# Performance work log

Hardware: AMD Instinct MI355X
Metric: run time of the kernel (lower is better)

The kernel has to match this reference:

```python
import jax, jax.numpy as jnp
import numpy as np

B, L, N, C = 64, 12, 4096, 3
FD, HD, OUT = 32, 64, 12
TID, DIW, TD = 288, 7, 16
STEPS = 4
EMB = 10  # node embedding dim for learned adjacency


def setup_inputs() -> dict:
    key = jax.random.key(0)
    ks = jax.random.split(key, 16)
    g = lambda i, shape, s=0.05: jax.random.normal(ks[i], shape, dtype=jnp.float32) * s
    z = lambda n: jnp.zeros((n,), jnp.float32)
    return {
        "history_data": jax.random.uniform(ks[0], (B, L, N, C), dtype=jnp.float32),
        "future_data": jnp.zeros((B, L, N, 1), jnp.float32),
        "batch_seen": 0,
        "epoch": 0,
        "train": 1,
        "tid_emb": g(1, (TID, TD)),
        "diw_emb": g(2, (DIW, TD)),
        "t2f_w": g(3, (2 * TD, FD)), "t2f_b": z(FD),
        "enc_w1": g(4, (L * C, HD)), "enc_b1": z(HD),
        "enc_w2": g(5, (HD, FD)), "enc_b2": z(FD),
        "node_emb": g(6, (N, EMB), 1.0),
        "pde_w1": g(7, (FD, HD)), "pde_b1": z(HD),
        "pde_w2": g(8, (HD, FD)), "pde_b2": z(FD),
        "ss_win": g(9, (FD, FD)), "ss_wst": g(10, (FD, FD)), "ss_b": z(FD),
        "ss_wout": g(11, (FD, FD)), "ss_bout": z(FD),
        "dec_w1": g(12, (FD, HD)), "dec_b1": z(HD),
        "dec_w2": g(13, (HD, OUT)), "dec_b2": z(OUT),
        "pde_mix": jnp.array(0.5, jnp.float32),
    }


def reference(history_data, future_data, batch_seen, epoch, train,
              tid_emb, diw_emb, t2f_w, t2f_b,
              enc_w1, enc_b1, enc_w2, enc_b2,
              node_emb,
              pde_w1, pde_b1, pde_w2, pde_b2,
              ss_win, ss_wst, ss_b, ss_wout, ss_bout,
              dec_w1, dec_b1, dec_w2, dec_b2, pde_mix):
    # --- encoder: per-node MLP over flattened (L, C) history ---
    x = history_data[..., :C]                                    # [B,L,N,C]
    x = jnp.transpose(x, (0, 2, 1, 3)).reshape(B, N, L * C)      # [B,N,L*C]
    field = jnp.maximum(x @ enc_w1 + enc_b1, 0.0) @ enc_w2 + enc_b2  # [B,N,FD]

    # --- temporal field bias from last-step tid/diw ---
    tid_idx = jnp.clip((history_data[:, -1, :, 1] * TID).astype(jnp.int32), 0, TID - 1)
    diw_idx = jnp.clip((history_data[:, -1, :, 2] * DIW).astype(jnp.int32), 0, DIW - 1)
    temp = jnp.concatenate([tid_emb[tid_idx], diw_emb[diw_idx]], axis=-1)  # [B,N,2*TD]
    field = field + temp @ t2f_w + t2f_b

    # --- learned adjacency for graph Laplacian (L = I - A) ---
    A = jax.nn.softmax(jnp.maximum(node_emb @ node_emb.T, 0.0), axis=-1)  # [N,N]

    alpha = jax.nn.sigmoid(pde_mix)
    dt = 1.0 / STEPS
    state = jnp.zeros_like(field)
    for _ in range(STEPS):  # fixed small unroll over PDE steps
        L_F = jnp.einsum('nm,bmf->bnf', A, field) - field         # (A - I) F
        N_F = jnp.maximum(field @ pde_w1 + pde_b1, 0.0) @ pde_w2 + pde_b2
        fe = field + (alpha * L_F + (1.0 - alpha) * N_F) * dt
        state = jnp.tanh(fe @ ss_win + state @ ss_wst + ss_b)     # state-space update
        field = fe + state @ ss_wout + ss_bout

    # --- decoder: per-node MLP to output horizon ---
    pred = jnp.maximum(field @ dec_w1 + dec_b1, 0.0) @ dec_w2 + dec_b2  # [B,N,OUT]
    return jnp.transpose(pred, (0, 2, 1))[..., None]              # [B,OUT,N,1]
```

## Files before the change

### kernel.cpp

```cpp
#include <hip/hip_runtime.h>

#define BATCH 64
#define LHIST 12
#define NNODE 4096
#define CCH   3
#define FD    32
#define HD    64
#define OUTD  12
#define TIDN  288
#define DIWN  7
#define TDD   16
#define EMBD  10
#define MROWS 2048
#define KDIM  4096
#define MTOT  (BATCH * NNODE)

typedef __attribute__((ext_vector_type(8))) short bf16x8;
typedef __attribute__((ext_vector_type(4))) float f32x4;

union BF8U { bf16x8 v; unsigned short s[8]; };

__device__ __forceinline__ unsigned short f2b(float f) {
    union { float f; unsigned u; } v; v.f = f;
    unsigned r = v.u + 0x7fffu + ((v.u >> 16) & 1u);
    return (unsigned short)(r >> 16);
}

__device__ __forceinline__ float b2f(unsigned short u) {
    union { unsigned u; float f; } v; v.u = (unsigned)u << 16; return v.f;
}

__device__ __forceinline__ float fast_tanh(float x) {
    x = fminf(fmaxf(x, -15.f), 15.f);
    const float e = __expf(2.f * x);
    return (e - 1.f) / (e + 1.f);
}

__device__ __forceinline__ bf16x8 ldsfrag(const unsigned short* p) {
    return *(const bf16x8*)p;
}

__device__ __forceinline__ bf16x8 pack8(float4 a, float4 b) {
    BF8U u;
    u.s[0] = f2b(a.x); u.s[1] = f2b(a.y); u.s[2] = f2b(a.z); u.s[3] = f2b(a.w);
    u.s[4] = f2b(b.x); u.s[5] = f2b(b.y); u.s[6] = f2b(b.z); u.s[7] = f2b(b.w);
    return u.v;
}

__global__ __launch_bounds__(256) void build_A(const float* __restrict__ emb,
                                               unsigned short* __restrict__ A) {
    const int n = blockIdx.x;
    const int tid = threadIdx.x;
    __shared__ float sc[NNODE];
    __shared__ float red[256];
    float e[EMBD];
#pragma unroll
    for (int c = 0; c < EMBD; c++) e[c] = emb[(size_t)n * EMBD + c];
    float mx = 0.f;
    for (int m = tid; m < NNODE; m += 256) {
        float s = 0.f;
#pragma unroll
        for (int c = 0; c < EMBD; c++) s += e[c] * emb[(size_t)m * EMBD + c];
        s = fmaxf(s, 0.f);
        sc[m] = s;
        mx = fmaxf(mx, s);
    }
    red[tid] = mx;
    __syncthreads();
    for (int off = 128; off > 0; off >>= 1) {
        if (tid < off) red[tid] = fmaxf(red[tid], red[tid + off]);
        __syncthreads();
    }
    mx = red[0];
    __syncthreads();
    float sum = 0.f;
    for (int m = tid; m < NNODE; m += 256) {
        float v = expf(sc[m] - mx);
        sc[m] = v;
        sum += v;
    }
    red[tid] = sum;
    __syncthreads();
    for (int off = 128; off > 0; off >>= 1) {
        if (tid < off) red[tid] += red[tid + off];
        __syncthreads();
    }
    const float inv = 1.f / red[0];
    for (int m = tid; m < NNODE; m += 256)
        A[(size_t)n * NNODE + m] = f2b(sc[m] * inv);
}

__global__ __launch_bounds__(256, 2) void encoder(const float* __restrict__ hist,
                                                  const float* __restrict__ tid_emb,
                                                  const float* __restrict__ diw_emb,
                                                  const float* __restrict__ t2f_w,
                                                  const float* __restrict__ t2f_b,
                                                  const float* __restrict__ enc_w1,
                                                  const float* __restrict__ enc_b1,
                                                  const float* __restrict__ enc_w2,
                                                  const float* __restrict__ enc_b2,
                                                  float* __restrict__ field,
                                                  unsigned short* __restrict__ fT) {
    const int gid = blockIdx.x * 256 + threadIdx.x;
    const int b = gid >> 12;
    const int n = gid & (NNODE - 1);
    const float* hb = hist + ((size_t)b * LHIST * NNODE + n) * CCH;
    float x[LHIST * CCH];
#pragma unroll
    for (int l = 0; l < LHIST; l++) {
        x[l * 3 + 0] = hb[(size_t)l * NNODE * CCH + 0];
        x[l * 3 + 1] = hb[(size_t)l * NNODE * CCH + 1];
        x[l * 3 + 2] = hb[(size_t)l * NNODE * CCH + 2];
    }
    float f[FD];
#pragma unroll
    for (int o = 0; o < FD; o++) f[o] = enc_b2[o] + t2f_b[o];
    for (int j = 0; j < HD; j++) {
        float h = enc_b1[j];
#pragma unroll
        for (int k = 0; k < LHIST * CCH; k++) h += x[k] * enc_w1[k * HD + j];
        h = fmaxf(h, 0.f);
#pragma unroll
        for (int o = 0; o < FD; o++) f[o] += h * enc_w2[j * FD + o];
    }
    const int ti = min(max((int)(x[11 * 3 + 1] * 288.0f), 0), TIDN - 1);
    const int di = min(max((int)(x[11 * 3 + 2] * 7.0f), 0), DIWN - 1);
    for (int g = 0; g < TDD; g++) {
        const float tg = tid_emb[ti * TDD + g];
        const float dg = diw_emb[di * TDD + g];
#pragma unroll
        for (int o = 0; o < FD; o++)
            f[o] += tg * t2f_w[g * FD + o] + dg * t2f_w[(TDD + g) * FD + o];
    }
#pragma unroll
    for (int o4 = 0; o4 < FD / 4; o4++) {
        float4 v = {f[o4 * 4 + 0], f[o4 * 4 + 1], f[o4 * 4 + 2], f[o4 * 4 + 3]};
        *(float4*)&field[(size_t)gid * FD + o4 * 4] = v;
    }
#pragma unroll
    for (int o = 0; o < FD; o++)
        fT[(size_t)(b * FD + o) * NNODE + n] = f2b(f[o]);
}

__global__ __launch_bounds__(256) void gemm_bt(const unsigned short* __restrict__ X,
                                               const unsigned short* __restrict__ Y,
                                               unsigned short* __restrict__ Cp) {
    constexpr int K = KDIM;
    constexpr int KS = KDIM / 2;
    constexpr int BK = 32;
    __shared__ __align__(16) unsigned short Xs[2][128 * BK];
    __shared__ __align__(16) unsigned short Ys[2][128 * BK];
    const int tid = threadIdx.x;
    const int wave = tid >> 6;
    const int lane = tid & 63;

    const int l = blockIdx.x + 16 * blockIdx.y;
    const int xcd = l & 7;
    const int rem = l >> 3;
    const int by = xcd * 4 + (rem & 3);
    const int bx = rem >> 2;
    const int i0 = bx * 128;
    const int j0 = by * 128;
    const int k0 = blockIdx.z * KS;
    unsigned short* C = Cp + (size_t)blockIdx.z * MTOT * FD;

    const int wi = (wave >> 1) * 64;
    const int wj = (wave & 1) * 64;

    const int lrow = lane >> 2;
    const int gcol = (lane & 3) * 8;
    const int scol = ((lane & 3) ^ ((lane >> 3) & 3)) * 8;

    const unsigned short* Xg = X + (size_t)(i0 + wave * 32 + lrow) * K + k0 + gcol;
    const unsigned short* Yg = Y + (size_t)(j0 + wave * 32 + lrow) * K + k0 + gcol;
    const int ldoff0 = (wave * 32 + lrow) * BK + scol;
    const int ldoff1 = (wave * 32 + 16 + lrow) * BK + scol;

    const f32x4 zero = {0.f, 0.f, 0.f, 0.f};
    f32x4 acc[4][4];
#pragma unroll
    for (int a = 0; a < 4; a++)
#pragma unroll
        for (int b = 0; b < 4; b++) acc[a][b] = zero;

    const int fr = lane & 15;
    const int q = lane >> 4;
    const int kq = (q ^ ((fr >> 1) & 3)) * 8;

    uint4 rx0 = *(const uint4*)(Xg);
    uint4 rx1 = *(const uint4*)(Xg + 16 * K);
    uint4 ry0 = *(const uint4*)(Yg);
    uint4 ry1 = *(const uint4*)(Yg + 16 * K);
    *(uint4*)&Xs[0][ldoff0] = rx0;
    *(uint4*)&Xs[0][ldoff1] = rx1;
    *(uint4*)&Ys[0][ldoff0] = ry0;
    *(uint4*)&Ys[0][ldoff1] = ry1;
    __syncthreads();

    int p = 0;
    for (int kt = 0; kt < KS; kt += BK) {
        const bool more = (kt + BK < KS);
        if (more) {
            rx0 = *(const uint4*)(Xg + kt + BK);
            rx1 = *(const uint4*)(Xg + kt + BK + 16 * K);
            ry0 = *(const uint4*)(Yg + kt + BK);
            ry1 = *(const uint4*)(Yg + kt + BK + 16 * K);
        }
        bf16x8 fa[4], fb[4];
#pragma unroll
        for (int t = 0; t < 4; t++)
            fa[t] = *(const bf16x8*)&Xs[p][(wi + t * 16 + fr) * BK + kq];
#pragma unroll
        for (int t = 0; t < 4; t++)
            fb[t] = *(const bf16x8*)&Ys[p][(wj + t * 16 + fr) * BK + kq];
#pragma unroll
        for (int mi = 0; mi < 4; mi++)
#pragma unroll
            for (int ni = 0; ni < 4; ni++)
                acc[mi][ni] = __builtin_amdgcn_mfma_f32_16x16x32_bf16(
                    fa[mi], fb[ni], acc[mi][ni], 0, 0, 0);
        if (more) {
            const int np = p ^ 1;
            *(uint4*)&Xs[np][ldoff0] = rx0;
            *(uint4*)&Xs[np][ldoff1] = rx1;
            *(uint4*)&Ys[np][ldoff0] = ry0;
            *(uint4*)&Ys[np][ldoff1] = ry1;
            __syncthreads();
            p = np;
        }
    }

    const int r0 = q * 4;
#pragma unroll
    for (int mi = 0; mi < 4; mi++) {
#pragma unroll
        for (int ni = 0; ni < 4; ni++) {
            const int R0 = i0 + wi + mi * 16 + r0;
            const int col = j0 + wj + ni * 16 + fr;
            const size_t addr = ((size_t)(R0 >> 5) * NNODE + col) * FD + (R0 & 31);
            ushort4 pk = {f2b(acc[mi][ni][0]), f2b(acc[mi][ni][1]),
                          f2b(acc[mi][ni][2]), f2b(acc[mi][ni][3])};
            *(ushort4*)&C[addr] = pk;
        }
    }
}

#define HPAD 72
#define FPAD 40
__global__ __launch_bounds__(256, 2) void step_mfma(const unsigned short* __restrict__ Ct0,
                                                    const unsigned short* __restrict__ Ct1,
                                                    float* __restrict__ field,
                                                    unsigned short* __restrict__ state,
                                                    unsigned short* __restrict__ fT,
                                                    const float* __restrict__ pde_w1,
                                                    const float* __restrict__ pde_b1,
                                                    const float* __restrict__ pde_w2,
                                                    const float* __restrict__ pde_b2,
                                                    const float* __restrict__ ss_win,
                                                    const float* __restrict__ ss_wst,
                                                    const float* __restrict__ ss_b,
                                                    const float* __restrict__ ss_wout,
                                                    const float* __restrict__ ss_bout,
                                                    const float* __restrict__ pde_mix,
                                                    const float* __restrict__ dec_w1,
                                                    const float* __restrict__ dec_b1,
                                                    const float* __restrict__ dec_w2,
                                                    const float* __restrict__ dec_b2,
                                                    float* __restrict__ out,
                                                    int first, int last) {
    __shared__ __align__(16) unsigned short W1T[HD * FD];
    __shared__ __align__(16) unsigned short W2T[FD * HD];
    __shared__ __align__(16) unsigned short WinT[FD * FD];
    __shared__ __align__(16) unsigned short WstT[FD * FD];
    __shared__ __align__(16) unsigned short WoutT[FD * FD];
    __shared__ __align__(16) unsigned short Wd1T[HD * FD];
    __shared__ __align__(16) unsigned short Wd2T[16 * HD];
    __shared__ __align__(16) unsigned short Hs[4 * 64 * HPAD];
    __shared__ __align__(16) unsigned short Fs[4 * 64 * FPAD];

    const int tid = threadIdx.x;
    for (int i = tid; i < HD * FD; i += 256) W1T[(i & 63) * FD + (i >> 6)] = f2b(pde_w1[i]);
    for (int i = tid; i < HD * FD; i += 256) W2T[(i & 31) * HD + (i >> 5)] = f2b(pde_w2[i]);
    for (int i = tid; i < FD * FD; i += 256) {
        WinT [(i & 31) * FD + (i >> 5)] = f2b(ss_win[i]);
        WstT [(i & 31) * FD + (i >> 5)] = f2b(ss_wst[i]);
        WoutT[(i & 31) * FD + (i >> 5)] = f2b(ss_wout[i]);
    }
    if (last) {
        for (int i = tid; i < HD * FD; i += 256)
            Wd1T[(i & 63) * FD + (i >> 6)] = f2b(dec_w1[i]);
        for (int i = tid; i < 16 * HD; i += 256) {
            const int o = i >> 6, j = i & 63;
            Wd2T[i] = (o < OUTD) ? f2b(dec_w2[j * OUTD + o]) : (unsigned short)0;
        }
    }
    __syncthreads();

    const int wv = tid >> 6;
    const int lane = tid & 63;
    const int ln = lane & 15;
    const int q = lane >> 4;
    const int kq = q * 8;
    const int r0 = q * 4;
    const int mw = blockIdx.x * 256 + wv * 64;
    const int b = mw >> 12;
    const int n0 = mw & (NNODE - 1);
    unsigned short* Hw = &Hs[wv * 64 * HPAD];
    unsigned short* Fw = &Fs[wv * 64 * FPAD];

    const float alpha = 1.f / (1.f + __expf(-pde_mix[0]));
    const float dt = 0.25f;

    bf16x8 w1f[4], w2f[2][2], winf[2], wstf[2], woutf[2];
#pragma unroll
    for (int nj = 0; nj < 4; nj++) w1f[nj] = ldsfrag(&W1T[(nj * 16 + ln) * FD + kq]);
#pragma unroll
    for (int nf = 0; nf < 2; nf++) {
#pragma unroll
        for (int kk = 0; kk < 2; kk++)
            w2f[nf][kk] = ldsfrag(&W2T[(nf * 16 + ln) * HD + kk * 32 + kq]);
        winf[nf]  = ldsfrag(&WinT [(nf * 16 + ln) * FD + kq]);
        wstf[nf]  = ldsfrag(&WstT [(nf * 16 + ln) * FD + kq]);
        woutf[nf] = ldsfrag(&WoutT[(nf * 16 + ln) * FD + kq]);
    }

    float b1v[4], b2v[2], bsv[2], bov[2];
#pragma unroll
    for (int nj = 0; nj < 4; nj++) b1v[nj] = pde_b1[nj * 16 + ln];
#pragma unroll
    for (int nf = 0; nf < 2; nf++) {
        b2v[nf] = pde_b2[nf * 16 + ln];
        bsv[nf] = ss_b[nf * 16 + ln];
        bov[nf] = ss_bout[nf * 16 + ln];
    }

    bf16x8 fA[4], stA[4];
#pragma unroll
    for (int mi = 0; mi < 4; mi++) {
        const float4* fp = (const float4*)&field[(size_t)(mw + mi * 16 + ln) * FD + kq];
        fA[mi] = pack8(fp[0], fp[1]);
    }
    if (!first) {
#pragma unroll
        for (int mi = 0; mi < 4; mi++)
            stA[mi] = *(const bf16x8*)&state[(size_t)(mw + mi * 16 + ln) * FD + kq];
    }

    const f32x4 zero = {0.f, 0.f, 0.f, 0.f};

    f32x4 hc[4][4];
#pragma unroll
    for (int mi = 0; mi < 4; mi++)
#pragma unroll
        for (int nj = 0; nj < 4; nj++)
            hc[mi][nj] = __builtin_amdgcn_mfma_f32_16x16x32_bf16(fA[mi], w1f[nj], zero, 0, 0, 0);
#pragma unroll
    for (int mi = 0; mi < 4; mi++)
#pragma unroll
        for (int nj = 0; nj < 4; nj++)
#pragma unroll
            for (int r = 0; r < 4; r++)
                Hw[(mi * 16 + r0 + r) * HPAD + nj * 16 + ln] =
                    f2b(fmaxf(hc[mi][nj][r] + b1v[nj], 0.f));

    float fld[4][2][4], ctv[4][2][4];
#pragma unroll
    for (int mi = 0; mi < 4; mi++)
#pragma unroll
        for (int nf = 0; nf < 2; nf++)
#pragma unroll
            for (int r = 0; r < 4; r++) {
                const size_t idx = (size_t)(mw + mi * 16 + r0 + r) * FD + nf * 16 + ln;
                fld[mi][nf][r] = field[idx];
                ctv[mi][nf][r] = b2f(Ct0[idx]) + b2f(Ct1[idx]);
            }

    bf16x8 hA[4][2];
#pragma unroll
    for (int mi = 0; mi < 4; mi++)
#pragma unroll
        for (int kk = 0; kk < 2; kk++)
            hA[mi][kk] = ldsfrag(&Hw[(mi * 16 + ln) * HPAD + kk * 32 + kq]);
    f32x4 nc[4][2];
#pragma unroll
    for (int mi = 0; mi < 4; mi++)
#pragma unroll
        for (int nf = 0; nf < 2; nf++) {
            f32x4 a = __builtin_amdgcn_mfma_f32_16x16x32_bf16(hA[mi][0], w2f[nf][0], zero, 0, 0, 0);
            nc[mi][nf] = __builtin_amdgcn_mfma_f32_16x16x32_bf16(hA[mi][1], w2f[nf][1], a, 0, 0, 0);
        }

    float fe[4][2][4];
#pragma unroll
    for (int mi = 0; mi < 4; mi++)
#pragma unroll
        for (int nf = 0; nf < 2; nf++)
#pragma unroll
            for (int r = 0; r < 4; r++) {
                const float nfv = nc[mi][nf][r] + b2v[nf];
                const float fv = fld[mi][nf][r];
                fe[mi][nf][r] = fv + (alpha * (ctv[mi][nf][r] - fv) + (1.f - alpha) * nfv) * dt;
                Fw[(mi * 16 + r0 + r) * FPAD + nf * 16 + ln] = f2b(fe[mi][nf][r]);
            }

    bf16x8 feA[4];
#pragma unroll
    for (int mi = 0; mi < 4; mi++) feA[mi] = ldsfrag(&Fw[(mi * 16 + ln) * FPAD + kq]);
    f32x4 sc_[4][2];
#pragma unroll
    for (int mi = 0; mi < 4; mi++)
#pragma unroll
        for (int nf = 0; nf < 2; nf++) {
            f32x4 a = __builtin_amdgcn_mfma_f32_16x16x32_bf16(feA[mi], winf[nf], zero, 0, 0, 0);
            if (!first)
                a = __builtin_amdgcn_mfma_f32_16x16x32_bf16(stA[mi], wstf[nf], a, 0, 0, 0);
            sc_[mi][nf] = a;
        }
    float sval[4][2][4];
#pragma unroll
    for (int mi = 0; mi < 4; mi++)
#pragma unroll
        for (int nf = 0; nf < 2; nf++)
#pragma unroll
            for (int r = 0; r < 4; r++)
                sval[mi][nf][r] = fast_tanh(sc_[mi][nf][r] + bsv[nf]);
#pragma unroll
    for (int mi = 0; mi < 4; mi++)
#pragma unroll
        for (int nf = 0; nf < 2; nf++)
#pragma unroll
            for (int r = 0; r < 4; r++)
                Fw[(mi * 16 + r0 + r) * FPAD + nf * 16 + ln] = f2b(sval[mi][nf][r]);

    bf16x8 SA[4];
#pragma unroll
    for (int mi = 0; mi < 4; mi++) SA[mi] = ldsfrag(&Fw[(mi * 16 + ln) * FPAD + kq]);
    float fnew[4][2][4];
#pragma unroll
    for (int mi = 0; mi < 4; mi++)
#pragma unroll
        for (int nf = 0; nf < 2; nf++) {
            f32x4 oc = __builtin_amdgcn_mfma_f32_16x16x32_bf16(SA[mi], woutf[nf], zero, 0, 0, 0);
#pragma unroll
            for (int r = 0; r < 4; r++)
                fnew[mi][nf][r] = fe[mi][nf][r] + oc[r] + bov[nf];
        }

    if (!last) {
#pragma unroll
        for (int mi = 0; mi < 4; mi++) {
#pragma unroll
            for (int nf = 0; nf < 2; nf++) {
#pragma unroll
                for (int r = 0; r < 4; r++) {
                    const size_t idx = (size_t)(mw + mi * 16 + r0 + r) * FD + nf * 16 + ln;
                    field[idx] = fnew[mi][nf][r];
                    state[idx] = f2b(sval[mi][nf][r]);
                }
                ushort4 pk = {f2b(fnew[mi][nf][0]), f2b(fnew[mi][nf][1]),
                              f2b(fnew[mi][nf][2]), f2b(fnew[mi][nf][3])};
                const size_t ft_addr = (size_t)(b * FD + nf * 16 + ln) * NNODE + n0 + mi * 16 + r0;
                *(ushort4*)&fT[ft_addr] = pk;
            }
        }
    } else {
        bf16x8 wd1f[4], wd2f[2];
#pragma unroll
        for (int nj = 0; nj < 4; nj++) wd1f[nj] = ldsfrag(&Wd1T[(nj * 16 + ln) * FD + kq]);
#pragma unroll
        for (int kk = 0; kk < 2; kk++) wd2f[kk] = ldsfrag(&Wd2T[ln * HD + kk * 32 + kq]);
        float db1v[4];
#pragma unroll
        for (int nj = 0; nj < 4; nj++) db1v[nj] = dec_b1[nj * 16 + ln];
        const float db2v = (ln < OUTD) ? dec_b2[ln] : 0.f;

#pragma unroll
        for (int mi = 0; mi < 4; mi++)
#pragma unroll
            for (int nf = 0; nf < 2; nf++)
#pragma unroll
                for (int r = 0; r < 4; r++)
                    Fw[(mi * 16 + r0 + r) * FPAD + nf * 16 + ln] = f2b(fnew[mi][nf][r]);
        bf16x8 fnA[4];
#pragma unroll
        for (int mi = 0; mi < 4; mi++) fnA[mi] = ldsfrag(&Fw[(mi * 16 + ln) * FPAD + kq]);

        f32x4 h2[4][4];
#pragma unroll
        for (int mi = 0; mi < 4; mi++)
#pragma unroll
            for (int nj = 0; nj < 4; nj++)
                h2[mi][nj] = __builtin_amdgcn_mfma_f32_16x16x32_bf16(fnA[mi], wd1f[nj], zero, 0, 0, 0);
#pragma unroll
        for (int mi = 0; mi < 4; mi++)
#pragma unroll
            for (int nj = 0; nj < 4; nj++)
#pragma unroll
                for (int r = 0; r < 4; r++)
                    Hw[(mi * 16 + r0 + r) * HPAD + nj * 16 + ln] =
                        f2b(fmaxf(h2[mi][nj][r] + db1v[nj], 0.f));
        bf16x8 h2A[4][2];
#pragma unroll
        for (int mi = 0; mi < 4; mi++)
#pragma unroll
            for (int kk = 0; kk < 2; kk++)
                h2A[mi][kk] = ldsfrag(&Hw[(mi * 16 + ln) * HPAD + kk * 32 + kq]);
#pragma unroll
        for (int mi = 0; mi < 4; mi++) {
            f32x4 a = __builtin_amdgcn_mfma_f32_16x16x32_bf16(h2A[mi][0], wd2f[0], zero, 0, 0, 0);
            a = __builtin_amdgcn_mfma_f32_16x16x32_bf16(h2A[mi][1], wd2f[1], a, 0, 0, 0);
            if (ln < OUTD) {
                float4 v = {a[0] + db2v, a[1] + db2v, a[2] + db2v, a[3] + db2v};
                *(float4*)&out[(size_t)(b * OUTD + ln) * NNODE + n0 + mi * 16 + r0] = v;
            }
        }
    }
}

extern "C" void kernel_launch(void* const* d_in, const int* in_sizes, int n_in,
                              void* d_out, int out_size, void* d_ws, size_t ws_size,
                              hipStream_t stream) {
    (void)in_sizes; (void)n_in; (void)out_size; (void)ws_size;
    const float* hist    = (const float*)d_in[0];
    const float* tid_emb = (const float*)d_in[5];
    const float* diw_emb = (const float*)d_in[6];
    const float* t2f_w   = (const float*)d_in[7];
    const float* t2f_b   = (const float*)d_in[8];
    const float* enc_w1  = (const float*)d_in[9];
    const float* enc_b1  = (const float*)d_in[10];
    const float* enc_w2  = (const float*)d_in[11];
    const float* enc_b2  = (const float*)d_in[12];
    const float* node_emb= (const float*)d_in[13];
    const float* pde_w1  = (const float*)d_in[14];
    const float* pde_b1  = (const float*)d_in[15];
    const float* pde_w2  = (const float*)d_in[16];
    const float* pde_b2  = (const float*)d_in[17];
    const float* ss_win  = (const float*)d_in[18];
    const float* ss_wst  = (const float*)d_in[19];
    const float* ss_b    = (const float*)d_in[20];
    const float* ss_wout = (const float*)d_in[21];
    const float* ss_bout = (const float*)d_in[22];
    const float* dec_w1  = (const float*)d_in[23];
    const float* dec_b1  = (const float*)d_in[24];
    const float* dec_w2  = (const float*)d_in[25];
    const float* dec_b2  = (const float*)d_in[26];
    const float* pde_mix = (const float*)d_in[27];

    char* w = (char*)d_ws;
    unsigned short* A_bf = (unsigned short*)w;  w += (size_t)KDIM * KDIM * 2;
    unsigned short* fT   = (unsigned short*)w;  w += (size_t)MROWS * KDIM * 2;
    float* field = (float*)w;                   w += (size_t)MTOT * FD * 4;
    unsigned short* state = (unsigned short*)w; w += (size_t)MTOT * FD * 2;
    unsigned short* Cp    = (unsigned short*)w; w += (size_t)2 * MTOT * FD * 2;

    build_A<<<NNODE, 256, 0, stream>>>(node_emb, A_bf);
    encoder<<<(BATCH * NNODE) / 256, 256, 0, stream>>>(hist, tid_emb, diw_emb, t2f_w,
                                                       t2f_b, enc_w1, enc_b1, enc_w2,
                                                       enc_b2, field, fT);
    for (int s = 0; s < 4; s++) {
        gemm_bt<<<dim3(16, 32, 2), 256, 0, stream>>>(fT, A_bf, Cp);
        step_mfma<<<MTOT / 256, 256, 0, stream>>>(
            Cp, Cp + (size_t)MTOT * FD, field, state, fT, pde_w1, pde_b1, pde_w2,
            pde_b2, ss_win, ss_wst, ss_b, ss_wout, ss_bout, pde_mix,
            dec_w1, dec_b1, dec_w2, dec_b2, (float*)d_out,
            s == 0 ? 1 : 0, s == 3 ? 1 : 0);
    }
}
```

Measured before the change: 732.0 us.

## Fuse graph GEMM with PDE step epilogue for first three steps

Adds a gemm_step kernel that computes the full-K A·F product for a 128x128 tile and runs the PDE/state-space update in its epilogue. The result is staged through shared memory instead of bf16 split-K partials in global memory, which removes a separate step kernel launch and the partial round trip for three of the four steps. fT is ping-ponged between two buffers because the fused kernel writes the next transposed field while other blocks still read the current one. The last step keeps split-K plus step_mfma with the decoder. The GEMM main loop is also unrolled by two with a deeper register prefetch. The costs are half as many blocks in the fused GEMM (no split-K), which may hurt occupancy, and a larger shared-memory footprint.

```diff
diff --git a/kernel.cpp b/kernel.cpp
--- a/kernel.cpp
+++ b/kernel.cpp
@@ -142,14 +142,318 @@
         fT[(size_t)(b * FD + o) * NNODE + n] = f2b(f[o]);
 }
 
+#define TPAD 36
+#define QHP  72
+#define QFP  40
+__global__ __launch_bounds__(256) void gemm_step(const unsigned short* __restrict__ X,
+                                                 const unsigned short* __restrict__ Y,
+                                                 float* __restrict__ field,
+                                                 unsigned short* __restrict__ state,
+                                                 unsigned short* __restrict__ fTo,
+                                                 const float* __restrict__ pde_w1,
+                                                 const float* __restrict__ pde_b1,
+                                                 const float* __restrict__ pde_w2,
+                                                 const float* __restrict__ pde_b2,
+                                                 const float* __restrict__ ss_win,
+                                                 const float* __restrict__ ss_wst,
+                                                 const float* __restrict__ ss_b,
+                                                 const float* __restrict__ ss_wout,
+                                                 const float* __restrict__ ss_bout,
+                                                 const float* __restrict__ pde_mix,
+                                                 int first) {
+    constexpr int K = KDIM;
+    constexpr int BK = 32;
+    __shared__ __align__(16) unsigned short SM0[512 * TPAD];
+    __shared__ __align__(16) unsigned short W1T[HD * FD];
+    __shared__ __align__(16) unsigned short W2T[FD * HD];
+    __shared__ __align__(16) unsigned short WinT[FD * FD];
+    __shared__ __align__(16) unsigned short WstT[FD * FD];
+    __shared__ __align__(16) unsigned short WoutT[FD * FD];
+    __shared__ __align__(16) unsigned short Hs[4 * 32 * QHP];
+    __shared__ __align__(16) unsigned short Fs[4 * 32 * QFP];
+
+    const int tid = threadIdx.x;
+    const int wave = tid >> 6;
+    const int lane = tid & 63;
+
+    for (int i = tid; i < HD * FD; i += 256) W1T[(i & 63) * FD + (i >> 6)] = f2b(pde_w1[i]);
+    for (int i = tid; i < HD * FD; i += 256) W2T[(i & 31) * HD + (i >> 5)] = f2b(pde_w2[i]);
+    for (int i = tid; i < FD * FD; i += 256) {
+        WinT [(i & 31) * FD + (i >> 5)] = f2b(ss_win[i]);
+        WstT [(i & 31) * FD + (i >> 5)] = f2b(ss_wst[i]);
+        WoutT[(i & 31) * FD + (i >> 5)] = f2b(ss_wout[i]);
+    }
+
+    const int l = blockIdx.x + 16 * blockIdx.y;
+    const int xcd = l & 7;
+    const int rem = l >> 3;
+    const int by = xcd * 4 + (rem & 3);
+    const int bx = rem >> 2;
+    const int i0 = bx * 128;
+    const int j0 = by * 128;
+    const int b0 = i0 >> 5;
+
+    const int wi = (wave >> 1) * 64;
+    const int wj = (wave & 1) * 64;
+
+    const int lrow = lane >> 2;
+    const int gcol = (lane & 3) * 8;
+    const int scol = ((lane & 3) ^ ((lane >> 3) & 3)) * 8;
+
+    const unsigned short* Xg = X + (size_t)(i0 + wave * 32 + lrow) * K + gcol;
+    const unsigned short* Yg = Y + (size_t)(j0 + wave * 32 + lrow) * K + gcol;
+    unsigned short* Xs = SM0;
+    unsigned short* Ys = SM0 + 8192;
+    const int ld0 = (wave * 32 + lrow) * BK + scol;
+    const int ld1 = (wave * 32 + 16 + lrow) * BK + scol;
+
+    const f32x4 zero = {0.f, 0.f, 0.f, 0.f};
+    f32x4 acc[4][4];
+#pragma unroll
+    for (int a = 0; a < 4; a++)
+#pragma unroll
+        for (int b = 0; b < 4; b++) acc[a][b] = zero;
+
+    const int fr = lane & 15;
+    const int q = lane >> 4;
+    const int kq8 = (q ^ ((fr >> 1) & 3)) * 8;
+
+#define GS_COMPUTE(P)                                                              \
+    {                                                                              \
+        bf16x8 fa[4], fb[4];                                                       \
+        _Pragma("unroll") for (int t = 0; t < 4; t++)                              \
+            fa[t] = *(const bf16x8*)&Xs[(P) * 4096 + (wi + t * 16 + fr) * BK + kq8]; \
+        _Pragma("unroll") for (int t = 0; t < 4; t++)                              \
+            fb[t] = *(const bf16x8*)&Ys[(P) * 4096 + (wj + t * 16 + fr) * BK + kq8]; \
+        _Pragma("unroll") for (int mi = 0; mi < 4; mi++)                           \
+            _Pragma("unroll") for (int ni = 0; ni < 4; ni++)                       \
+                acc[mi][ni] = __builtin_amdgcn_mfma_f32_16x16x32_bf16(             \
+                    fa[mi], fb[ni], acc[mi][ni], 0, 0, 0);                         \
+    }
+
+    uint4 ax0 = *(const uint4*)(Xg);
+    uint4 ax1 = *(const uint4*)(Xg + 16 * K);
+    uint4 ay0 = *(const uint4*)(Yg);
+    uint4 ay1 = *(const uint4*)(Yg + 16 * K);
+    uint4 bx0 = *(const uint4*)(Xg + BK);
+    uint4 bx1 = *(const uint4*)(Xg + BK + 16 * K);
+    uint4 by0 = *(const uint4*)(Yg + BK);
+    uint4 by1 = *(const uint4*)(Yg + BK + 16 * K);
+    *(uint4*)&Xs[ld0] = ax0; *(uint4*)&Xs[ld1] = ax1;
+    *(uint4*)&Ys[ld0] = ay0; *(uint4*)&Ys[ld1] = ay1;
+    __syncthreads();
+
+    int p = 0;
+    for (int kt = 0; kt < K; kt += 2 * BK) {
+        if (kt + 2 * BK < K) {
+            ax0 = *(const uint4*)(Xg + kt + 2 * BK);
+            ax1 = *(const uint4*)(Xg + kt + 2 * BK + 16 * K);
+            ay0 = *(const uint4*)(Yg + kt + 2 * BK);
+            ay1 = *(const uint4*)(Yg + kt + 2 * BK + 16 * K);
+        }
+        GS_COMPUTE(p);
+        {
+            const int np = p ^ 1;
+            *(uint4*)&Xs[np * 4096 + ld0] = bx0; *(uint4*)&Xs[np * 4096 + ld1] = bx1;
+            *(uint4*)&Ys[np * 4096 + ld0] = by0; *(uint4*)&Ys[np * 4096 + ld1] = by1;
+            __syncthreads();
+        }
+        if (kt + 3 * BK < K) {
+            bx0 = *(const uint4*)(Xg + kt + 3 * BK);
+            bx1 = *(const uint4*)(Xg + kt + 3 * BK + 16 * K);
+            by0 = *(const uint4*)(Yg + kt + 3 * BK);
+            by1 = *(const uint4*)(Yg + kt + 3 * BK + 16 * K);
+        }
+        GS_COMPUTE(p ^ 1);
+        if (kt + 2 * BK < K) {
+            *(uint4*)&Xs[p * 4096 + ld0] = ax0; *(uint4*)&Xs[p * 4096 + ld1] = ax1;
+            *(uint4*)&Ys[p * 4096 + ld0] = ay0; *(uint4*)&Ys[p * 4096 + ld1] = ay1;
+            __syncthreads();
+        }
+    }
+#undef GS_COMPUTE
+
+    __syncthreads();
+    unsigned short* T = SM0;
+    const int r0 = q * 4;
+#pragma unroll
+    for (int mi = 0; mi < 4; mi++) {
+#pragma unroll
+        for (int ni = 0; ni < 4; ni++) {
+            const int R0 = i0 + wi + mi * 16 + r0;
+            const int nl = wj + ni * 16 + fr;
+            ushort4 pk = {f2b(acc[mi][ni][0]), f2b(acc[mi][ni][1]),
+                          f2b(acc[mi][ni][2]), f2b(acc[mi][ni][3])};
+            *(ushort4*)&T[((((R0 >> 5) & 3) << 7) + nl) * TPAD + (R0 & 31)] = pk;
+        }
+    }
+    __syncthreads();
+
+    const int ln = fr;
+    const int kq = q * 8;
+    unsigned short* Hw = &Hs[wave * 32 * QHP];
+    unsigned short* Fw = &Fs[wave * 32 * QFP];
+    const float alpha = 1.f / (1.f + __expf(-pde_mix[0]));
+    const float dt = 0.25f;
+
+    bf16x8 w1f[4], w2f[2][2], winf[2], wstf[2], woutf[2];
+#pragma unroll
+    for (int nj = 0; nj < 4; nj++) w1f[nj] = ldsfrag(&W1T[(nj * 16 + ln) * FD + kq]);
+#pragma unroll
+    for (int nf = 0; nf < 2; nf++) {
+#pragma unroll
+        for (int kk = 0; kk < 2; kk++)
+            w2f[nf][kk] = ldsfrag(&W2T[(nf * 16 + ln) * HD + kk * 32 + kq]);
+        winf[nf]  = ldsfrag(&WinT [(nf * 16 + ln) * FD + kq]);
+        wstf[nf]  = ldsfrag(&WstT [(nf * 16 + ln) * FD + kq]);
+        woutf[nf] = ldsfrag(&WoutT[(nf * 16 + ln) * FD + kq]);
+    }
+    float b1v[4], b2v[2], bsv[2], bov[2];
+#pragma unroll
+    for (int nj = 0; nj < 4; nj++) b1v[nj] = pde_b1[nj * 16 + ln];
+#pragma unroll
+    for (int nf = 0; nf < 2; nf++) {
+        b2v[nf] = pde_b2[nf * 16 + ln];
+        bsv[nf] = ss_b[nf * 16 + ln];
+        bov[nf] = ss_bout[nf * 16 + ln];
+    }
+
+    for (int qtr = 0; qtr < 4; qtr++) {
+        const int lb = wave * 128 + qtr * 32;
+        const int bb = lb >> 7;
+        const int nl0 = lb & 127;
+        const int bg = b0 + bb;
+        const int mwg = (bg << 12) + j0 + nl0;
+
+        bf16x8 fA[2], stA[2];
+#pragma unroll
+        for (int mi = 0; mi < 2; mi++) {
+            const float4* fp = (const float4*)&field[(size_t)(mwg + mi * 16 + ln) * FD + kq];
+            fA[mi] = pack8(fp[0], fp[1]);
+        }
+        if (!first) {
+#pragma unroll
+            for (int mi = 0; mi < 2; mi++)
+                stA[mi] = *(const bf16x8*)&state[(size_t)(mwg + mi * 16 + ln) * FD + kq];
+        }
+
+        f32x4 hc[2][4];
+#pragma unroll
+        for (int mi = 0; mi < 2; mi++)
+#pragma unroll
+            for (int nj = 0; nj < 4; nj++)
+                hc[mi][nj] = __builtin_amdgcn_mfma_f32_16x16x32_bf16(fA[mi], w1f[nj], zero, 0, 0, 0);
+#pragma unroll
+        for (int mi = 0; mi < 2; mi++)
+#pragma unroll
+            for (int nj = 0; nj < 4; nj++)
+#pragma unroll
+                for (int r = 0; r < 4; r++)
+                    Hw[(mi * 16 + r0 + r) * QHP + nj * 16 + ln] =
+                        f2b(fmaxf(hc[mi][nj][r] + b1v[nj], 0.f));
+
+        float fld[2][2][4], ctv[2][2][4];
+#pragma unroll
+        for (int mi = 0; mi < 2; mi++)
+#pragma unroll
+            for (int nf = 0; nf < 2; nf++)
+#pragma unroll
+                for (int r = 0; r < 4; r++) {
+                    const size_t idx = (size_t)(mwg + mi * 16 + r0 + r) * FD + nf * 16 + ln;
+                    fld[mi][nf][r] = field[idx];
+                    ctv[mi][nf][r] = b2f(T[(lb + mi * 16 + r0 + r) * TPAD + nf * 16 + ln]);
+                }
+
+        bf16x8 hA[2][2];
+#pragma unroll
+        for (int mi = 0; mi < 2; mi++)
+#pragma unroll
+            for (int kk = 0; kk < 2; kk++)
+                hA[mi][kk] = ldsfrag(&Hw[(mi * 16 + ln) * QHP + kk * 32 + kq]);
+        f32x4 nc[2][2];
+#pragma unroll
+        for (int mi = 0; mi < 2; mi++)
+#pragma unroll
+            for (int nf = 0; nf < 2; nf++) {
+                f32x4 a = __builtin_amdgcn_mfma_f32_16x16x32_bf16(hA[mi][0], w2f[nf][0], zero, 0, 0, 0);
+                nc[mi][nf] = __builtin_amdgcn_mfma_f32_16x16x32_bf16(hA[mi][1], w2f[nf][1], a, 0, 0, 0);
+            }
+
+        float fe[2][2][4];
+#pragma unroll
+        for (int mi = 0; mi < 2; mi++)
+#pragma unroll
+            for (int nf = 0; nf < 2; nf++)
+#pragma unroll
+                for (int r = 0; r < 4; r++) {
+                    const float nfv = nc[mi][nf][r] + b2v[nf];
+                    const float fv = fld[mi][nf][r];
+                    fe[mi][nf][r] = fv + (alpha * (ctv[mi][nf][r] - fv) + (1.f - alpha) * nfv) * dt;
+                    Fw[(mi * 16 + r0 + r) * QFP + nf * 16 + ln] = f2b(fe[mi][nf][r]);
+                }
+
+        bf16x8 feA[2];
+#pragma unroll
+        for (int mi = 0; mi < 2; mi++) feA[mi] = ldsfrag(&Fw[(mi * 16 + ln) * QFP + kq]);
+        f32x4 sc_[2][2];
+#pragma unroll
+        for (int mi = 0; mi < 2; mi++)
+#pragma unroll
+            for (int nf = 0; nf < 2; nf++) {
+                f32x4 a = __builtin_amdgcn_mfma_f32_16x16x32_bf16(feA[mi], winf[nf], zero, 0, 0, 0);
+                if (!first)
+                    a = __builtin_amdgcn_mfma_f32_16x16x32_bf16(stA[mi], wstf[nf], a, 0, 0, 0);
+                sc_[mi][nf] = a;
+            }
+        float sval[2][2][4];
+#pragma unroll
+        for (int mi = 0; mi < 2; mi++)
+#pragma unroll
+            for (int nf = 0; nf < 2; nf++)
+#pragma unroll
+                for (int r = 0; r < 4; r++)
+                    sval[mi][nf][r] = fast_tanh(sc_[mi][nf][r] + bsv[nf]);
+#pragma unroll
+        for (int mi = 0; mi < 2; mi++)
+#pragma unroll
+            for (int nf = 0; nf < 2; nf++)
+#pragma unroll
+                for (int r = 0; r < 4; r++)
+                    Fw[(mi * 16 + r0 + r) * QFP + nf * 16 + ln] = f2b(sval[mi][nf][r]);
+
+        bf16x8 SA[2];
+#pragma unroll
+        for (int mi = 0; mi < 2; mi++) SA[mi] = ldsfrag(&Fw[(mi * 16 + ln) * QFP + kq]);
+#pragma unroll
+        for (int mi = 0; mi < 2; mi++) {
+#pragma unroll
+            for (int nf = 0; nf < 2; nf++) {
+                f32x4 oc = __builtin_amdgcn_mfma_f32_16x16x32_bf16(SA[mi], woutf[nf], zero, 0, 0, 0);
+                float fnew[4];
+#pragma unroll
+                for (int r = 0; r < 4; r++) {
+                    fnew[r] = fe[mi][nf][r] + oc[r] + bov[nf];
+                    const size_t idx = (size_t)(mwg + mi * 16 + r0 + r) * FD + nf * 16 + ln;
+                    field[idx] = fnew[r];
+                    state[idx] = f2b(sval[mi][nf][r]);
+                }
+                ushort4 pk = {f2b(fnew[0]), f2b(fnew[1]), f2b(fnew[2]), f2b(fnew[3])};
+                const size_t fta = (size_t)(bg * FD + nf * 16 + ln) * NNODE
+                                 + j0 + nl0 + mi * 16 + r0;
+                *(ushort4*)&fTo[fta] = pk;
+            }
+        }
+    }
+}
+
 __global__ __launch_bounds__(256) void gemm_bt(const unsigned short* __restrict__ X,
                                                const unsigned short* __restrict__ Y,
                                                unsigned short* __restrict__ Cp) {
     constexpr int K = KDIM;
     constexpr int KS = KDIM / 2;
     constexpr int BK = 32;
-    __shared__ __align__(16) unsigned short Xs[2][128 * BK];
-    __shared__ __align__(16) unsigned short Ys[2][128 * BK];
+    __shared__ __align__(16) unsigned short Xs[2 * 4096];
+    __shared__ __align__(16) unsigned short Ys[2 * 4096];
     const int tid = threadIdx.x;
     const int wave = tid >> 6;
     const int lane = tid & 63;
@@ -173,8 +477,8 @@
 
     const unsigned short* Xg = X + (size_t)(i0 + wave * 32 + lrow) * K + k0 + gcol;
     const unsigned short* Yg = Y + (size_t)(j0 + wave * 32 + lrow) * K + k0 + gcol;
-    const int ldoff0 = (wave * 32 + lrow) * BK + scol;
-    const int ldoff1 = (wave * 32 + 16 + lrow) * BK + scol;
+    const int ld0 = (wave * 32 + lrow) * BK + scol;
+    const int ld1 = (wave * 32 + 16 + lrow) * BK + scol;
 
     const f32x4 zero = {0.f, 0.f, 0.f, 0.f};
     f32x4 acc[4][4];
@@ -185,50 +489,62 @@
 
     const int fr = lane & 15;
     const int q = lane >> 4;
-    const int kq = (q ^ ((fr >> 1) & 3)) * 8;
-
-    uint4 rx0 = *(const uint4*)(Xg);
-    uint4 rx1 = *(const uint4*)(Xg + 16 * K);
-    uint4 ry0 = *(const uint4*)(Yg);
-    uint4 ry1 = *(const uint4*)(Yg + 16 * K);
-    *(uint4*)&Xs[0][ldoff0] = rx0;
-    *(uint4*)&Xs[0][ldoff1] = rx1;
-    *(uint4*)&Ys[0][ldoff0] = ry0;
-    *(uint4*)&Ys[0][ldoff1] = ry1;
+    const int kq8 = (q ^ ((fr >> 1) & 3)) * 8;
+
+#define GB_COMPUTE(P)                                                              \
+    {                                                                              \
+        bf16x8 fa[4], fb[4];                                                       \
+        _Pragma("unroll") for (int t = 0; t < 4; t++)                              \
+            fa[t] = *(const bf16x8*)&Xs[(P) * 4096 + (wi + t * 16 + fr) * BK + kq8]; \
+        _Pragma("unroll") for (int t = 0; t < 4; t++)                              \
+            fb[t] = *(const bf16x8*)&Ys[(P) * 4096 + (wj + t * 16 + fr) * BK + kq8]; \
+        _Pragma("unroll") for (int mi = 0; mi < 4; mi++)                           \
+            _Pragma("unroll") for (int ni = 0; ni < 4; ni++)                       \
+                acc[mi][ni] = __builtin_amdgcn_mfma_f32_16x16x32_bf16(             \
+                    fa[mi], fb[ni], acc[mi][ni], 0, 0, 0);                         \
+    }
+
+    uint4 ax0 = *(const uint4*)(Xg);
+    uint4 ax1 = *(const uint4*)(Xg + 16 * K);
+    uint4 ay0 = *(const uint4*)(Yg);
+    uint4 ay1 = *(const uint4*)(Yg + 16 * K);
+    uint4 bx0 = *(const uint4*)(Xg + BK);
+    uint4 bx1 = *(const uint4*)(Xg + BK + 16 * K);
+    uint4 by0 = *(const uint4*)(Yg + BK);
+    uint4 by1 = *(const uint4*)(Yg + BK + 16 * K);
+    *(uint4*)&Xs[ld0] = ax0; *(uint4*)&Xs[ld1] = ax1;
+    *(uint4*)&Ys[ld0] = ay0; *(uint4*)&Ys[ld1] = ay1;
     __syncthreads();
 
     int p = 0;
-    for (int kt = 0; kt < KS; kt += BK) {
-        const bool more = (kt + BK < KS);
-        if (more) {
-            rx0 = *(const uint4*)(Xg + kt + BK);
-            rx1 = *(const uint4*)(Xg + kt + BK + 16 * K);
-            ry0 = *(const uint4*)(Yg + kt + BK);
-            ry1 = *(const uint4*)(Yg + kt + BK + 16 * K);
-        }
-        bf16x8 fa[4], fb[4];
-#pragma unroll
-        for (int t = 0; t < 4; t++)
-            fa[t] = *(const bf16x8*)&Xs[p][(wi + t * 16 + fr) * BK + kq];
-#pragma unroll
-        for (int t = 0; t < 4; t++)
-            fb[t] = *(const bf16x8*)&Ys[p][(wj + t * 16 + fr) * BK + kq];
-#pragma unroll
-        for (int mi = 0; mi < 4; mi++)
-#pragma unroll
-            for (int ni = 0; ni < 4; ni++)
-                acc[mi][ni] = __builtin_amdgcn_mfma_f32_16x16x32_bf16(
-                    fa[mi], fb[ni], acc[mi][ni], 0, 0, 0);
-        if (more) {
+    for (int kt = 0; kt < KS; kt += 2 * BK) {
+        if (kt + 2 * BK < KS) {
+            ax0 = *(const uint4*)(Xg + kt + 2 * BK);
+            ax1 = *(const uint4*)(Xg + kt + 2 * BK + 16 * K);
+            ay0 = *(const uint4*)(Yg + kt + 2 * BK);
+            ay1 = *(const uint4*)(Yg + kt + 2 * BK + 16 * K);
+        }
+        GB_COMPUTE(p);
+        {
             const int np = p ^ 1;
-            *(uint4*)&Xs[np][ldoff0] = rx0;
-            *(uint4*)&Xs[np][ldoff1] = rx1;
-            *(uint4*)&Ys[np][ldoff0] = ry0;
-            *(uint4*)&Ys[np][ldoff1] = ry1;
+            *(uint4*)&Xs[np * 4096 + ld0] = bx0; *(uint4*)&Xs[np * 4096 + ld1] = bx1;
+            *(uint4*)&Ys[np * 4096 + ld0] = by0; *(uint4*)&Ys[np * 4096 + ld1] = by1;
             __syncthreads();
-            p = np;
-        }
-    }
+        }
+        if (kt + 3 * BK < KS) {
+            bx0 = *(const uint4*)(Xg + kt + 3 * BK);
+            bx1 = *(const uint4*)(Xg + kt + 3 * BK + 16 * K);
+            by0 = *(const uint4*)(Yg + kt + 3 * BK);
+            by1 = *(const uint4*)(Yg + kt + 3 * BK + 16 * K);
+        }
+        GB_COMPUTE(p ^ 1);
+        if (kt + 2 * BK < KS) {
+            *(uint4*)&Xs[p * 4096 + ld0] = ax0; *(uint4*)&Xs[p * 4096 + ld1] = ax1;
+            *(uint4*)&Ys[p * 4096 + ld0] = ay0; *(uint4*)&Ys[p * 4096 + ld1] = ay1;
+            __syncthreads();
+        }
+    }
+#undef GB_COMPUTE
 
     const int r0 = q * 4;
 #pragma unroll
@@ -251,7 +567,6 @@
                                                     const unsigned short* __restrict__ Ct1,
                                                     float* __restrict__ field,
                                                     unsigned short* __restrict__ state,
-                                                    unsigned short* __restrict__ fT,
                                                     const float* __restrict__ pde_w1,
                                                     const float* __restrict__ pde_b1,
                                                     const float* __restrict__ pde_w2,
@@ -266,8 +581,7 @@
                                                     const float* __restrict__ dec_b1,
                                                     const float* __restrict__ dec_w2,
                                                     const float* __restrict__ dec_b2,
-                                                    float* __restrict__ out,
-                                                    int first, int last) {
+                                                    float* __restrict__ out) {
     __shared__ __align__(16) unsigned short W1T[HD * FD];
     __shared__ __align__(16) unsigned short W2T[FD * HD];
     __shared__ __align__(16) unsigned short WinT[FD * FD];
@@ -286,13 +600,11 @@
         WstT [(i & 31) * FD + (i >> 5)] = f2b(ss_wst[i]);
         WoutT[(i & 31) * FD + (i >> 5)] = f2b(ss_wout[i]);
     }
-    if (last) {
-        for (int i = tid; i < HD * FD; i += 256)
-            Wd1T[(i & 63) * FD + (i >> 6)] = f2b(dec_w1[i]);
-        for (int i = tid; i < 16 * HD; i += 256) {
-            const int o = i >> 6, j = i & 63;
-            Wd2T[i] = (o < OUTD) ? f2b(dec_w2[j * OUTD + o]) : (unsigned short)0;
-        }
+    for (int i = tid; i < HD * FD; i += 256)
+        Wd1T[(i & 63) * FD + (i >> 6)] = f2b(dec_w1[i]);
+    for (int i = tid; i < 16 * HD; i += 256) {
+        const int o = i >> 6, j = i & 63;
+        Wd2T[i] = (o < OUTD) ? f2b(dec_w2[j * OUTD + o]) : (unsigned short)0;
     }
     __syncthreads();
 
@@ -340,11 +652,9 @@
         const float4* fp = (const float4*)&field[(size_t)(mw + mi * 16 + ln) * FD + kq];
         fA[mi] = pack8(fp[0], fp[1]);
     }
-    if (!first) {
-#pragma unroll
-        for (int mi = 0; mi < 4; mi++)
-            stA[mi] = *(const bf16x8*)&state[(size_t)(mw + mi * 16 + ln) * FD + kq];
-    }
+#pragma unroll
+    for (int mi = 0; mi < 4; mi++)
+        stA[mi] = *(const bf16x8*)&state[(size_t)(mw + mi * 16 + ln) * FD + kq];
 
     const f32x4 zero = {0.f, 0.f, 0.f, 0.f};
 
@@ -412,8 +722,7 @@
 #pragma unroll
         for (int nf = 0; nf < 2; nf++) {
             f32x4 a = __builtin_amdgcn_mfma_f32_16x16x32_bf16(feA[mi], winf[nf], zero, 0, 0, 0);
-            if (!first)
-                a = __builtin_amdgcn_mfma_f32_16x16x32_bf16(stA[mi], wstf[nf], a, 0, 0, 0);
+            a = __builtin_amdgcn_mfma_f32_16x16x32_bf16(stA[mi], wstf[nf], a, 0, 0, 0);
             sc_[mi][nf] = a;
         }
     float sval[4][2][4];
@@ -446,73 +755,54 @@
                 fnew[mi][nf][r] = fe[mi][nf][r] + oc[r] + bov[nf];
         }
 
-    if (!last) {
-#pragma unroll
-        for (int mi = 0; mi < 4; mi++) {
-#pragma unroll
-            for (int nf = 0; nf < 2; nf++) {
-#pragma unroll
-                for (int r = 0; r < 4; r++) {
-                    const size_t idx = (size_t)(mw + mi * 16 + r0 + r) * FD + nf * 16 + ln;
-                    field[idx] = fnew[mi][nf][r];
-                    state[idx] = f2b(sval[mi][nf][r]);
-                }
-                ushort4 pk = {f2b(fnew[mi][nf][0]), f2b(fnew[mi][nf][1]),
-                              f2b(fnew[mi][nf][2]), f2b(fnew[mi][nf][3])};
-                const size_t ft_addr = (size_t)(b * FD + nf * 16 + ln) * NNODE + n0 + mi * 16 + r0;
-                *(ushort4*)&fT[ft_addr] = pk;
-            }
-        }
-    } else {
-        bf16x8 wd1f[4], wd2f[2];
-#pragma unroll
-        for (int nj = 0; nj < 4; nj++) wd1f[nj] = ldsfrag(&Wd1T[(nj * 16 + ln) * FD + kq]);
-#pragma unroll
-        for (int kk = 0; kk < 2; kk++) wd2f[kk] = ldsfrag(&Wd2T[ln * HD + kk * 32 + kq]);
-        float db1v[4];
-#pragma unroll
-        for (int nj = 0; nj < 4; nj++) db1v[nj] = dec_b1[nj * 16 + ln];
-        const float db2v = (ln < OUTD) ? dec_b2[ln] : 0.f;
-
-#pragma unroll
-        for (int mi = 0; mi < 4; mi++)
-#pragma unroll
-            for (int nf = 0; nf < 2; nf++)
-#pragma unroll
-                for (int r = 0; r < 4; r++)
-                    Fw[(mi * 16 + r0 + r) * FPAD + nf * 16 + ln] = f2b(fnew[mi][nf][r]);
-        bf16x8 fnA[4];
-#pragma unroll
-        for (int mi = 0; mi < 4; mi++) fnA[mi] = ldsfrag(&Fw[(mi * 16 + ln) * FPAD + kq]);
-
-        f32x4 h2[4][4];
-#pragma unroll
-        for (int mi = 0; mi < 4; mi++)
-#pragma unroll
-            for (int nj = 0; nj < 4; nj++)
-                h2[mi][nj] = __builtin_amdgcn_mfma_f32_16x16x32_bf16(fnA[mi], wd1f[nj], zero, 0, 0, 0);
-#pragma unroll
-        for (int mi = 0; mi < 4; mi++)
-#pragma unroll
-            for (int nj = 0; nj < 4; nj++)
-#pragma unroll
-                for (int r = 0; r < 4; r++)
-                    Hw[(mi * 16 + r0 + r) * HPAD + nj * 16 + ln] =
-                        f2b(fmaxf(h2[mi][nj][r] + db1v[nj], 0.f));
-        bf16x8 h2A[4][2];
-#pragma unroll
-        for (int mi = 0; mi < 4; mi++)
-#pragma unroll
-            for (int kk = 0; kk < 2; kk++)
-                h2A[mi][kk] = ldsfrag(&Hw[(mi * 16 + ln) * HPAD + kk * 32 + kq]);
-#pragma unroll
-        for (int mi = 0; mi < 4; mi++) {
-            f32x4 a = __builtin_amdgcn_mfma_f32_16x16x32_bf16(h2A[mi][0], wd2f[0], zero, 0, 0, 0);
-            a = __builtin_amdgcn_mfma_f32_16x16x32_bf16(h2A[mi][1], wd2f[1], a, 0, 0, 0);
-            if (ln < OUTD) {
-                float4 v = {a[0] + db2v, a[1] + db2v, a[2] + db2v, a[3] + db2v};
-                *(float4*)&out[(size_t)(b * OUTD + ln) * NNODE + n0 + mi * 16 + r0] = v;
-            }
+    bf16x8 wd1f[4], wd2f[2];
+#pragma unroll
+    for (int nj = 0; nj < 4; nj++) wd1f[nj] = ldsfrag(&Wd1T[(nj * 16 + ln) * FD + kq]);
+#pragma unroll
+    for (int kk = 0; kk < 2; kk++) wd2f[kk] = ldsfrag(&Wd2T[ln * HD + kk * 32 + kq]);
+    float db1v[4];
+#pragma unroll
+    for (int nj = 0; nj < 4; nj++) db1v[nj] = dec_b1[nj * 16 + ln];
+    const float db2v = (ln < OUTD) ? dec_b2[ln] : 0.f;
+
+#pragma unroll
+    for (int mi = 0; mi < 4; mi++)
+#pragma unroll
+        for (int nf = 0; nf < 2; nf++)
+#pragma unroll
+            for (int r = 0; r < 4; r++)
+                Fw[(mi * 16 + r0 + r) * FPAD + nf * 16 + ln] = f2b(fnew[mi][nf][r]);
+    bf16x8 fnA[4];
+#pragma unroll
+    for (int mi = 0; mi < 4; mi++) fnA[mi] = ldsfrag(&Fw[(mi * 16 + ln) * FPAD + kq]);
+
+    f32x4 h2[4][4];
+#pragma unroll
+    for (int mi = 0; mi < 4; mi++)
+#pragma unroll
+        for (int nj = 0; nj < 4; nj++)
+            h2[mi][nj] = __builtin_amdgcn_mfma_f32_16x16x32_bf16(fnA[mi], wd1f[nj], zero, 0, 0, 0);
+#pragma unroll
+    for (int mi = 0; mi < 4; mi++)
+#pragma unroll
+        for (int nj = 0; nj < 4; nj++)
+#pragma unroll
+            for (int r = 0; r < 4; r++)
+                Hw[(mi * 16 + r0 + r) * HPAD + nj * 16 + ln] =
+                    f2b(fmaxf(h2[mi][nj][r] + db1v[nj], 0.f));
+    bf16x8 h2A[4][2];
+#pragma unroll
+    for (int mi = 0; mi < 4; mi++)
+#pragma unroll
+        for (int kk = 0; kk < 2; kk++)
+            h2A[mi][kk] = ldsfrag(&Hw[(mi * 16 + ln) * HPAD + kk * 32 + kq]);
+#pragma unroll
+    for (int mi = 0; mi < 4; mi++) {
+        f32x4 a = __builtin_amdgcn_mfma_f32_16x16x32_bf16(h2A[mi][0], wd2f[0], zero, 0, 0, 0);
+        a = __builtin_amdgcn_mfma_f32_16x16x32_bf16(h2A[mi][1], wd2f[1], a, 0, 0, 0);
+        if (ln < OUTD) {
+            float4 v = {a[0] + db2v, a[1] + db2v, a[2] + db2v, a[3] + db2v};
+            *(float4*)&out[(size_t)(b * OUTD + ln) * NNODE + n0 + mi * 16 + r0] = v;
         }
     }
 }
@@ -548,7 +838,8 @@
 
     char* w = (char*)d_ws;
     unsigned short* A_bf = (unsigned short*)w;  w += (size_t)KDIM * KDIM * 2;
-    unsigned short* fT   = (unsigned short*)w;  w += (size_t)MROWS * KDIM * 2;
+    unsigned short* fTa  = (unsigned short*)w;  w += (size_t)MROWS * KDIM * 2;
+    unsigned short* fTb  = (unsigned short*)w;  w += (size_t)MROWS * KDIM * 2;
     float* field = (float*)w;                   w += (size_t)MTOT * FD * 4;
     unsigned short* state = (unsigned short*)w; w += (size_t)MTOT * FD * 2;
     unsigned short* Cp    = (unsigned short*)w; w += (size_t)2 * MTOT * FD * 2;
@@ -556,13 +847,16 @@
     build_A<<<NNODE, 256, 0, stream>>>(node_emb, A_bf);
     encoder<<<(BATCH * NNODE) / 256, 256, 0, stream>>>(hist, tid_emb, diw_emb, t2f_w,
                                                        t2f_b, enc_w1, enc_b1, enc_w2,
-                                                       enc_b2, field, fT);
-    for (int s = 0; s < 4; s++) {
-        gemm_bt<<<dim3(16, 32, 2), 256, 0, stream>>>(fT, A_bf, Cp);
-        step_mfma<<<MTOT / 256, 256, 0, stream>>>(
-            Cp, Cp + (size_t)MTOT * FD, field, state, fT, pde_w1, pde_b1, pde_w2,
-            pde_b2, ss_win, ss_wst, ss_b, ss_wout, ss_bout, pde_mix,
-            dec_w1, dec_b1, dec_w2, dec_b2, (float*)d_out,
-            s == 0 ? 1 : 0, s == 3 ? 1 : 0);
-    }
-}
+                                                       enc_b2, field, fTa);
+    unsigned short* fts[4] = {fTa, fTb, fTa, fTb};
+    for (int s = 0; s < 3; s++) {
+        gemm_step<<<dim3(16, 32), 256, 0, stream>>>(
+            fts[s], A_bf, field, state, fts[s + 1], pde_w1, pde_b1, pde_w2, pde_b2,
+            ss_win, ss_wst, ss_b, ss_wout, ss_bout, pde_mix, s == 0 ? 1 : 0);
+    }
+    gemm_bt<<<dim3(16, 32, 2), 256, 0, stream>>>(fts[3], A_bf, Cp);
+    step_mfma<<<MTOT / 256, 256, 0, stream>>>(
+        Cp, Cp + (size_t)MTOT * FD, field, state, pde_w1, pde_b1, pde_w2, pde_b2,
+        ss_win, ss_wst, ss_b, ss_wout, ss_bout, pde_mix,
+        dec_w1, dec_b1, dec_w2, dec_b2, (float*)d_out);
+}
```

Measured after the change: 683.5 us. 6.6% less time.
